# Optimization experiments

Hardware: AMD Instinct MI355X
Metric: run time of the kernel (lower is better)

Reference implementation:

```python
import jax, jax.numpy as jnp
import numpy as np

VOCAB = 1_000_000   # vocabulary_size
EMBED = 128         # embedding_size
BATCH = 4096
NUM_SAMPLED = 8192  # negative_samples


def setup_inputs() -> dict:
    key = jax.random.key(0)
    k1, k2, k3, k4 = jax.random.split(key, 4)
    predictions = jax.random.normal(k1, (BATCH, EMBED), dtype=jnp.float32)
    labels = jax.random.randint(k2, (BATCH, 1), 0, VOCAB, dtype=jnp.int64)
    # TF draws these via log_uniform_candidate_sampler; here they are fixed inputs.
    sampled_ids = jax.random.randint(k3, (NUM_SAMPLED,), 0, VOCAB, dtype=jnp.int64)
    W = jax.random.normal(k4, (VOCAB, EMBED), dtype=jnp.float32) * 0.05  # glorot-ish scale
    b = jnp.zeros((VOCAB,), dtype=jnp.float32)
    return {"predictions": predictions, "labels": labels,
            "sampled_ids": sampled_ids, "W": W, "b": b}


def _log_uniform_prob(ids, vocab):
    # P(k) = (log(k+2) - log(k+1)) / log(vocab+1), TF's log-uniform sampler.
    k = ids.astype(jnp.float32)
    return (jnp.log(k + 2.0) - jnp.log(k + 1.0)) / jnp.log(float(vocab) + 1.0)


def reference(predictions, labels, sampled_ids, W, b):
    lbl = labels[:, 0]                                   # [B]
    # --- true logits: gather one row per example ---
    true_w = W[lbl]                                      # [B, D] gather
    true_logits = jnp.sum(predictions * true_w, axis=-1) + b[lbl]
    true_logits = true_logits - jnp.log(NUM_SAMPLED * _log_uniform_prob(lbl, VOCAB))
    # --- sampled logits: gather S rows, small GEMM ---
    sampled_w = W[sampled_ids]                           # [S, D] gather
    sampled_logits = jnp.einsum('bd,sd->bs', predictions, sampled_w) + b[sampled_ids]
    sampled_logits = sampled_logits - jnp.log(NUM_SAMPLED * _log_uniform_prob(sampled_ids, VOCAB))
    # --- softmax cross-entropy with true class at column 0 ---
    logits = jnp.concatenate([true_logits[:, None], sampled_logits], axis=1)  # [B, 1+S]
    per_example_loss = -jax.nn.log_softmax(logits, axis=-1)[:, 0]
    return jnp.mean(per_example_loss)
```

## Files before the change

kernel.cpp:

```cpp
#include <hip/hip_runtime.h>
#include <hip/hip_bf16.h>
#include <math.h>

#define M 4096
#define N 8192
#define K 128
#define NSAMP 8192
#define VOCABF 1000000.0f

typedef __bf16 bf16x8 __attribute__((ext_vector_type(8)));
typedef float f32x16 __attribute__((ext_vector_type(16)));
typedef unsigned short u16x8 __attribute__((ext_vector_type(8)));

__device__ inline unsigned short f2bf(float f) {
    unsigned int u = __float_as_uint(f);
    unsigned int r = (u + 0x7FFFu + ((u >> 16) & 1u)) >> 16;
    return (unsigned short)r;
}

__global__ __launch_bounds__(256) void prep(const float* __restrict__ pred,
                                            const int* __restrict__ sampled,
                                            const float* __restrict__ W,
                                            const float* __restrict__ bias,
                                            unsigned short* __restrict__ Pb,
                                            unsigned short* __restrict__ Wsb,
                                            float* __restrict__ bcorr,
                                            float* __restrict__ rsum,
                                            float* __restrict__ out) {
    const int bx = blockIdx.x;
    if (bx < 256) {
        int t = bx * 256 + threadIdx.x;
        if (t < M) rsum[t] = 0.0f;
        if (t == 0) out[0] = 0.0f;
        int base = t * 8;
        float4 f0 = *(const float4*)(pred + base);
        float4 f1 = *(const float4*)(pred + base + 4);
        u16x8 v;
        v[0] = f2bf(f0.x); v[1] = f2bf(f0.y); v[2] = f2bf(f0.z); v[3] = f2bf(f0.w);
        v[4] = f2bf(f1.x); v[5] = f2bf(f1.y); v[6] = f2bf(f1.z); v[7] = f2bf(f1.w);
        *(u16x8*)(Pb + base) = v;
    } else {
        int t = (bx - 256) * 256 + threadIdx.x;
        int s = t >> 4, c = t & 15;
        int id = sampled[s];
        const float* src = W + (size_t)id * K + c * 8;
        float4 f0 = *(const float4*)src;
        float4 f1 = *(const float4*)(src + 4);
        u16x8 v;
        v[0] = f2bf(f0.x); v[1] = f2bf(f0.y); v[2] = f2bf(f0.z); v[3] = f2bf(f0.w);
        v[4] = f2bf(f1.x); v[5] = f2bf(f1.y); v[6] = f2bf(f1.z); v[7] = f2bf(f1.w);
        *(u16x8*)(Wsb + s * K + c * 8) = v;
        if (c == 0) {
            float kk = (float)id;
            float q = log1pf(1.0f / (kk + 1.0f)) / logf(VOCABF + 1.0f);
            bcorr[s] = bias[id] - logf((float)NSAMP * q);
        }
    }
}

__global__ __launch_bounds__(256, 4) void main_gemm(
        const unsigned short* __restrict__ Pb,
        const unsigned short* __restrict__ Wsb,
        const float* __restrict__ bcorr,
        float* __restrict__ row_sum) {
    const int tid  = threadIdx.x;
    const int lane = tid & 63;
    const int wid  = tid >> 6;
    const int l31  = lane & 31;
    const int half = lane >> 5;
    const int mrow = blockIdx.x * 128 + wid * 32 + l31;
    const int nb   = blockIdx.y * 256;

    bf16x8 a[8];
    const unsigned short* ap = Pb + (size_t)mrow * K + half * 8;
#pragma unroll
    for (int ks = 0; ks < 8; ++ks)
        a[ks] = *(const bf16x8*)(ap + ks * 16);

    float rs[16];
#pragma unroll
    for (int r = 0; r < 16; ++r) rs[r] = 0.0f;

#pragma unroll
    for (int t = 0; t < 8; ++t) {
        const int col = nb + t * 32 + l31;
        const float bc = bcorr[col];
        f32x16 acc;
#pragma unroll
        for (int r = 0; r < 16; ++r) acc[r] = bc;
        const unsigned short* bp = Wsb + (size_t)col * K + half * 8;
#pragma unroll
        for (int ks = 0; ks < 8; ++ks) {
            bf16x8 bf = *(const bf16x8*)(bp + ks * 16);
            acc = __builtin_amdgcn_mfma_f32_32x32x16_bf16(a[ks], bf, acc, 0, 0, 0);
        }
#pragma unroll
        for (int r = 0; r < 16; ++r) rs[r] += __expf(acc[r]);
    }

#pragma unroll
    for (int m = 1; m <= 16; m <<= 1) {
#pragma unroll
        for (int r = 0; r < 16; ++r) rs[r] += __shfl_xor(rs[r], m, 64);
    }
    if (l31 == 0) {
        const int rb = blockIdx.x * 128 + wid * 32 + 4 * half;
#pragma unroll
        for (int r = 0; r < 16; ++r) {
            int row = rb + (r & 3) + 8 * (r >> 2);
            atomicAdd(&row_sum[row], rs[r]);
        }
    }
}

__global__ __launch_bounds__(256) void finalize(const float* __restrict__ pred,
                                                const int* __restrict__ labels,
                                                const float* __restrict__ W,
                                                const float* __restrict__ bias,
                                                const float* __restrict__ row_sum,
                                                float* __restrict__ out) {
    __shared__ float part[16];
    int t = blockIdx.x * 256 + threadIdx.x;
    int row = t >> 4, c = t & 15;
    int id = labels[row];
    const float* wp = W + (size_t)id * K + c * 8;
    const float* pp = pred + (size_t)row * K + c * 8;
    float4 w0 = *(const float4*)wp, w1 = *(const float4*)(wp + 4);
    float4 p0 = *(const float4*)pp, p1 = *(const float4*)(pp + 4);
    float d = w0.x * p0.x + w0.y * p0.y + w0.z * p0.z + w0.w * p0.w
            + w1.x * p1.x + w1.y * p1.y + w1.z * p1.z + w1.w * p1.w;
#pragma unroll
    for (int m = 1; m <= 8; m <<= 1) d += __shfl_xor(d, m, 64);
    if (c == 0) {
        float kk = (float)id;
        float q = log1pf(1.0f / (kk + 1.0f)) / logf(VOCABF + 1.0f);
        float tl = d + bias[id] - logf((float)NSAMP * q);
        float loss = logf(row_sum[row] + __expf(tl)) - tl;
        part[threadIdx.x >> 4] = loss;
    }
    __syncthreads();
    if (threadIdx.x == 0) {
        float s = 0.0f;
#pragma unroll
        for (int i = 0; i < 16; ++i) s += part[i];
        atomicAdd(out, s * (1.0f / (float)M));
    }
}

extern "C" void kernel_launch(void* const* d_in, const int* in_sizes, int n_in,
                              void* d_out, int out_size, void* d_ws, size_t ws_size,
                              hipStream_t stream) {
    const float* pred    = (const float*)d_in[0];
    const int*   labels  = (const int*)d_in[1];
    const int*   sampled = (const int*)d_in[2];
    const float* W       = (const float*)d_in[3];
    const float* b       = (const float*)d_in[4];
    float* out = (float*)d_out;

    char* ws = (char*)d_ws;
    unsigned short* Wsb   = (unsigned short*)ws;
    unsigned short* Pb    = (unsigned short*)(ws + (1 << 21));
    float*          bcorr = (float*)(ws + (1 << 21) + (1 << 20));
    float*          rsum  = (float*)(ws + (1 << 21) + (1 << 20) + NSAMP * 4);

    prep<<<768, 256, 0, stream>>>(pred, sampled, W, b, Pb, Wsb, bcorr, rsum, out);
    main_gemm<<<dim3(32, 32), 256, 0, stream>>>(Pb, Wsb, bcorr, rsum);
    finalize<<<256, 256, 0, stream>>>(pred, labels, W, b, rsum, out);
}
```

Before: 594.6 us.

## Fuse prep into GEMM with double-buffered LDS staging and atomic-free partial sums

Removes the separate prep kernel. The GEMM now converts predictions to bf16 in registers and gathers the sampled W rows directly, staging them into swizzled, double-buffered shared memory with the bias correction computed per tile. Row-sum atomics are replaced by per-column-block partial writes that finalize reduces, which drops the zeroing pass. In exchange, each of the 32 column-block rows of workgroups re-gathers and re-converts the same W rows, and every workgroup converts its own copy of the prediction tile. There is also an extra barrier per tile iteration.

New measurement: 631.5 us. 1.06x slower.

```diff
diff --git a/kernel.cpp b/kernel.cpp
--- a/kernel.cpp
+++ b/kernel.cpp
@@ -3,9 +3,8 @@
 #include <math.h>
 
 #define M 4096
-#define N 8192
+#define NSAMP 8192
 #define K 128
-#define NSAMP 8192
 #define VOCABF 1000000.0f
 
 typedef __bf16 bf16x8 __attribute__((ext_vector_type(8)));
@@ -14,88 +13,102 @@
 
 __device__ inline unsigned short f2bf(float f) {
     unsigned int u = __float_as_uint(f);
-    unsigned int r = (u + 0x7FFFu + ((u >> 16) & 1u)) >> 16;
-    return (unsigned short)r;
+    return (unsigned short)((u + 0x7FFFu + ((u >> 16) & 1u)) >> 16);
 }
 
-__global__ __launch_bounds__(256) void prep(const float* __restrict__ pred,
-                                            const int* __restrict__ sampled,
-                                            const float* __restrict__ W,
-                                            const float* __restrict__ bias,
-                                            unsigned short* __restrict__ Pb,
-                                            unsigned short* __restrict__ Wsb,
-                                            float* __restrict__ bcorr,
-                                            float* __restrict__ rsum,
-                                            float* __restrict__ out) {
-    const int bx = blockIdx.x;
-    if (bx < 256) {
-        int t = bx * 256 + threadIdx.x;
-        if (t < M) rsum[t] = 0.0f;
-        if (t == 0) out[0] = 0.0f;
-        int base = t * 8;
-        float4 f0 = *(const float4*)(pred + base);
-        float4 f1 = *(const float4*)(pred + base + 4);
-        u16x8 v;
-        v[0] = f2bf(f0.x); v[1] = f2bf(f0.y); v[2] = f2bf(f0.z); v[3] = f2bf(f0.w);
-        v[4] = f2bf(f1.x); v[5] = f2bf(f1.y); v[6] = f2bf(f1.z); v[7] = f2bf(f1.w);
-        *(u16x8*)(Pb + base) = v;
-    } else {
-        int t = (bx - 256) * 256 + threadIdx.x;
-        int s = t >> 4, c = t & 15;
-        int id = sampled[s];
-        const float* src = W + (size_t)id * K + c * 8;
-        float4 f0 = *(const float4*)src;
-        float4 f1 = *(const float4*)(src + 4);
-        u16x8 v;
-        v[0] = f2bf(f0.x); v[1] = f2bf(f0.y); v[2] = f2bf(f0.z); v[3] = f2bf(f0.w);
-        v[4] = f2bf(f1.x); v[5] = f2bf(f1.y); v[6] = f2bf(f1.z); v[7] = f2bf(f1.w);
-        *(u16x8*)(Wsb + s * K + c * 8) = v;
-        if (c == 0) {
-            float kk = (float)id;
-            float q = log1pf(1.0f / (kk + 1.0f)) / logf(VOCABF + 1.0f);
-            bcorr[s] = bias[id] - logf((float)NSAMP * q);
-        }
-    }
+__device__ inline u16x8 pack8(float4 f0, float4 f1) {
+    u16x8 v;
+    v[0] = f2bf(f0.x); v[1] = f2bf(f0.y); v[2] = f2bf(f0.z); v[3] = f2bf(f0.w);
+    v[4] = f2bf(f1.x); v[5] = f2bf(f1.y); v[6] = f2bf(f1.z); v[7] = f2bf(f1.w);
+    return v;
+}
+__device__ inline bf16x8 as_bf(u16x8 u) {
+    union { u16x8 u; bf16x8 b; } cv; cv.u = u; return cv.b;
 }
 
-__global__ __launch_bounds__(256, 4) void main_gemm(
-        const unsigned short* __restrict__ Pb,
-        const unsigned short* __restrict__ Wsb,
-        const float* __restrict__ bcorr,
-        float* __restrict__ row_sum) {
+__global__ __launch_bounds__(256, 4) void fused_gemm(
+        const float* __restrict__ pred,
+        const int* __restrict__ sampled,
+        const float* __restrict__ W,
+        const float* __restrict__ bias,
+        float* __restrict__ partial,
+        float* __restrict__ out) {
+    __shared__ __align__(16) unsigned short Bt[2][32 * K];
+    __shared__ float Bc[2][32];
+
     const int tid  = threadIdx.x;
     const int lane = tid & 63;
     const int wid  = tid >> 6;
     const int l31  = lane & 31;
     const int half = lane >> 5;
-    const int mrow = blockIdx.x * 128 + wid * 32 + l31;
-    const int nb   = blockIdx.y * 256;
+    const int bx = blockIdx.x, by = blockIdx.y;
 
+    if (bx == 0 && by == 0 && tid == 0) out[0] = 0.0f;
+
+    const int mrow = bx * 128 + wid * 32 + l31;
     bf16x8 a[8];
-    const unsigned short* ap = Pb + (size_t)mrow * K + half * 8;
+    {
+        const float* ap = pred + (size_t)mrow * K + half * 8;
 #pragma unroll
-    for (int ks = 0; ks < 8; ++ks)
-        a[ks] = *(const bf16x8*)(ap + ks * 16);
+        for (int ks = 0; ks < 8; ++ks) {
+            float4 f0 = *(const float4*)(ap + ks * 16);
+            float4 f1 = *(const float4*)(ap + ks * 16 + 4);
+            a[ks] = as_bf(pack8(f0, f1));
+        }
+    }
+
+    const int scol = tid >> 3;
+    const int seg  = tid & 7;
+    float4 r0, r1, r2, r3; float bsv = 0.0f; int sid = 0;
+
+    auto LOAD = [&](int t) {
+        sid = sampled[by * 256 + t * 32 + scol];
+        const float4* src = (const float4*)(W + (size_t)sid * K + seg * 16);
+        r0 = src[0]; r1 = src[1]; r2 = src[2]; r3 = src[3];
+        if (seg == 0) bsv = bias[sid];
+    };
+    auto WRITE = [&](int b) {
+        u16x8 lo = pack8(r0, r1), hi = pack8(r2, r3);
+        const int swz = (scol & 15) << 4;
+        char* rowp = (char*)&Bt[b][scol * K];
+        const int o0 = seg * 32;
+        *(u16x8*)(rowp + ((o0)      ^ swz)) = lo;
+        *(u16x8*)(rowp + ((o0 + 16) ^ swz)) = hi;
+        if (seg == 0) {
+            float kk = (float)sid;
+            float q = log1pf(1.0f / (kk + 1.0f)) / logf(VOCABF + 1.0f);
+            Bc[b][scol] = bsv - logf((float)NSAMP * q);
+        }
+    };
 
     float rs[16];
 #pragma unroll
     for (int r = 0; r < 16; ++r) rs[r] = 0.0f;
 
+    LOAD(0); WRITE(0);
+    __syncthreads();
+
 #pragma unroll
     for (int t = 0; t < 8; ++t) {
-        const int col = nb + t * 32 + l31;
-        const float bc = bcorr[col];
+        const int cur = t & 1;
+        if (t < 7) LOAD(t + 1);
+
+        const float bc = Bc[cur][l31];
         f32x16 acc;
 #pragma unroll
         for (int r = 0; r < 16; ++r) acc[r] = bc;
-        const unsigned short* bp = Wsb + (size_t)col * K + half * 8;
+        const char* rowp = (const char*)&Bt[cur][l31 * K];
+        const int swz = (l31 & 15) << 4;
 #pragma unroll
         for (int ks = 0; ks < 8; ++ks) {
-            bf16x8 bf = *(const bf16x8*)(bp + ks * 16);
+            bf16x8 bf = *(const bf16x8*)(rowp + ((half * 16 + ks * 32) ^ swz));
             acc = __builtin_amdgcn_mfma_f32_32x32x16_bf16(a[ks], bf, acc, 0, 0, 0);
         }
 #pragma unroll
         for (int r = 0; r < 16; ++r) rs[r] += __expf(acc[r]);
+
+        if (t < 7) WRITE((t + 1) & 1);
+        __syncthreads();
     }
 
 #pragma unroll
@@ -104,11 +117,11 @@
         for (int r = 0; r < 16; ++r) rs[r] += __shfl_xor(rs[r], m, 64);
     }
     if (l31 == 0) {
-        const int rb = blockIdx.x * 128 + wid * 32 + 4 * half;
+        const int rb = bx * 128 + wid * 32 + 4 * half;
 #pragma unroll
         for (int r = 0; r < 16; ++r) {
             int row = rb + (r & 3) + 8 * (r >> 2);
-            atomicAdd(&row_sum[row], rs[r]);
+            partial[by * M + row] = rs[r];
         }
     }
 }
@@ -117,7 +130,7 @@
                                                 const int* __restrict__ labels,
                                                 const float* __restrict__ W,
                                                 const float* __restrict__ bias,
-                                                const float* __restrict__ row_sum,
+                                                const float* __restrict__ partial,
                                                 float* __restrict__ out) {
     __shared__ float part[16];
     int t = blockIdx.x * 256 + threadIdx.x;
@@ -129,21 +142,25 @@
     float4 p0 = *(const float4*)pp, p1 = *(const float4*)(pp + 4);
     float d = w0.x * p0.x + w0.y * p0.y + w0.z * p0.z + w0.w * p0.w
             + w1.x * p1.x + w1.y * p1.y + w1.z * p1.z + w1.w * p1.w;
+    float s = partial[c * M + row] + partial[(c + 16) * M + row];
 #pragma unroll
-    for (int m = 1; m <= 8; m <<= 1) d += __shfl_xor(d, m, 64);
+    for (int m = 1; m <= 8; m <<= 1) {
+        d += __shfl_xor(d, m, 64);
+        s += __shfl_xor(s, m, 64);
+    }
     if (c == 0) {
         float kk = (float)id;
         float q = log1pf(1.0f / (kk + 1.0f)) / logf(VOCABF + 1.0f);
         float tl = d + bias[id] - logf((float)NSAMP * q);
-        float loss = logf(row_sum[row] + __expf(tl)) - tl;
+        float loss = logf(s + __expf(tl)) - tl;
         part[threadIdx.x >> 4] = loss;
     }
     __syncthreads();
     if (threadIdx.x == 0) {
-        float s = 0.0f;
+        float sum = 0.0f;
 #pragma unroll
-        for (int i = 0; i < 16; ++i) s += part[i];
-        atomicAdd(out, s * (1.0f / (float)M));
+        for (int i = 0; i < 16; ++i) sum += part[i];
+        atomicAdd(out, sum * (1.0f / (float)M));
     }
 }
 
@@ -157,13 +174,8 @@
     const float* b       = (const float*)d_in[4];
     float* out = (float*)d_out;
 
-    char* ws = (char*)d_ws;
-    unsigned short* Wsb   = (unsigned short*)ws;
-    unsigned short* Pb    = (unsigned short*)(ws + (1 << 21));
-    float*          bcorr = (float*)(ws + (1 << 21) + (1 << 20));
-    float*          rsum  = (float*)(ws + (1 << 21) + (1 << 20) + NSAMP * 4);
+    float* partial = (float*)d_ws;
 
-    prep<<<768, 256, 0, stream>>>(pred, sampled, W, b, Pb, Wsb, bcorr, rsum, out);
-    main_gemm<<<dim3(32, 32), 256, 0, stream>>>(Pb, Wsb, bcorr, rsum);
-    finalize<<<256, 256, 0, stream>>>(pred, labels, W, b, rsum, out);
+    fused_gemm<<<dim3(32, 32), 256, 0, stream>>>(pred, sampled, W, b, partial, out);
+    finalize<<<256, 256, 0, stream>>>(pred, labels, W, b, partial, out);
 }
```

## Fuse pred conversion into GEMM, move true-logit into prep, replace atomics with partials

Applied to the files above, without the earlier changes.

Drops the separate bf16 conversion of predictions: the GEMM now loads fp32 predictions and converts them in registers. The true-logit dot product moves into the prep kernel alongside the sampled-row gather. Per-row atomicAdds in the GEMM are replaced by plain stores into a per-column-block partial buffer, which a smaller finalize kernel reduces. This removes atomic contention and the workspace round trip for the converted predictions, at the cost of twice the fp32 reads for A in the GEMM and a 32-way partial reduction.

Measured after the change: 597.5 us. No clear change (+0.5%).

```diff
diff --git a/kernel.cpp b/kernel.cpp
--- a/kernel.cpp
+++ b/kernel.cpp
@@ -3,9 +3,8 @@
 #include <math.h>
 
 #define M 4096
-#define N 8192
+#define NSAMP 8192
 #define K 128
-#define NSAMP 8192
 #define VOCABF 1000000.0f
 
 typedef __bf16 bf16x8 __attribute__((ext_vector_type(8)));
@@ -14,55 +13,69 @@
 
 __device__ inline unsigned short f2bf(float f) {
     unsigned int u = __float_as_uint(f);
-    unsigned int r = (u + 0x7FFFu + ((u >> 16) & 1u)) >> 16;
-    return (unsigned short)r;
+    return (unsigned short)((u + 0x7FFFu + ((u >> 16) & 1u)) >> 16);
+}
+
+__device__ inline u16x8 pack8(float4 f0, float4 f1) {
+    u16x8 v;
+    v[0] = f2bf(f0.x); v[1] = f2bf(f0.y); v[2] = f2bf(f0.z); v[3] = f2bf(f0.w);
+    v[4] = f2bf(f1.x); v[5] = f2bf(f1.y); v[6] = f2bf(f1.z); v[7] = f2bf(f1.w);
+    return v;
+}
+__device__ inline bf16x8 as_bf(u16x8 u) {
+    union { u16x8 u; bf16x8 b; } cv; cv.u = u; return cv.b;
 }
 
 __global__ __launch_bounds__(256) void prep(const float* __restrict__ pred,
+                                            const int* __restrict__ labels,
                                             const int* __restrict__ sampled,
                                             const float* __restrict__ W,
                                             const float* __restrict__ bias,
-                                            unsigned short* __restrict__ Pb,
                                             unsigned short* __restrict__ Wsb,
                                             float* __restrict__ bcorr,
-                                            float* __restrict__ rsum,
+                                            float* __restrict__ tl,
                                             float* __restrict__ out) {
+    const float inv_logv = 1.0f / logf(VOCABF + 1.0f);
     const int bx = blockIdx.x;
-    if (bx < 256) {
+    if (bx < 512) {
         int t = bx * 256 + threadIdx.x;
-        if (t < M) rsum[t] = 0.0f;
         if (t == 0) out[0] = 0.0f;
-        int base = t * 8;
-        float4 f0 = *(const float4*)(pred + base);
-        float4 f1 = *(const float4*)(pred + base + 4);
-        u16x8 v;
-        v[0] = f2bf(f0.x); v[1] = f2bf(f0.y); v[2] = f2bf(f0.z); v[3] = f2bf(f0.w);
-        v[4] = f2bf(f1.x); v[5] = f2bf(f1.y); v[6] = f2bf(f1.z); v[7] = f2bf(f1.w);
-        *(u16x8*)(Pb + base) = v;
-    } else {
-        int t = (bx - 256) * 256 + threadIdx.x;
         int s = t >> 4, c = t & 15;
         int id = sampled[s];
         const float* src = W + (size_t)id * K + c * 8;
         float4 f0 = *(const float4*)src;
         float4 f1 = *(const float4*)(src + 4);
-        u16x8 v;
-        v[0] = f2bf(f0.x); v[1] = f2bf(f0.y); v[2] = f2bf(f0.z); v[3] = f2bf(f0.w);
-        v[4] = f2bf(f1.x); v[5] = f2bf(f1.y); v[6] = f2bf(f1.z); v[7] = f2bf(f1.w);
-        *(u16x8*)(Wsb + s * K + c * 8) = v;
+        *(u16x8*)(Wsb + s * K + c * 8) = pack8(f0, f1);
         if (c == 0) {
             float kk = (float)id;
-            float q = log1pf(1.0f / (kk + 1.0f)) / logf(VOCABF + 1.0f);
+            float q = log1pf(1.0f / (kk + 1.0f)) * inv_logv;
             bcorr[s] = bias[id] - logf((float)NSAMP * q);
+        }
+    } else {
+        int t = (bx - 512) * 256 + threadIdx.x;
+        int row = t >> 4, c = t & 15;
+        int id = labels[row];
+        const float* wp = W + (size_t)id * K + c * 8;
+        const float* pp = pred + (size_t)row * K + c * 8;
+        float4 w0 = *(const float4*)wp, w1 = *(const float4*)(wp + 4);
+        float4 p0 = *(const float4*)pp, p1 = *(const float4*)(pp + 4);
+        float d = w0.x * p0.x + w0.y * p0.y + w0.z * p0.z + w0.w * p0.w
+                + w1.x * p1.x + w1.y * p1.y + w1.z * p1.z + w1.w * p1.w;
+#pragma unroll
+        for (int m = 1; m <= 8; m <<= 1) d += __shfl_xor(d, m, 64);
+        if (c == 0) {
+            float kk = (float)id;
+            float q = log1pf(1.0f / (kk + 1.0f)) * inv_logv;
+            tl[row] = d + bias[id] - logf((float)NSAMP * q);
         }
     }
 }
 
 __global__ __launch_bounds__(256, 4) void main_gemm(
-        const unsigned short* __restrict__ Pb,
+        const float* __restrict__ pred,
         const unsigned short* __restrict__ Wsb,
         const float* __restrict__ bcorr,
-        float* __restrict__ row_sum) {
+        float* __restrict__ partial) {
     const int tid  = threadIdx.x;
     const int lane = tid & 63;
     const int wid  = tid >> 6;
@@ -72,10 +85,15 @@
     const int nb   = blockIdx.y * 256;
 
     bf16x8 a[8];
-    const unsigned short* ap = Pb + (size_t)mrow * K + half * 8;
+    {
+        const float* ap = pred + (size_t)mrow * K + half * 8;
 #pragma unroll
-    for (int ks = 0; ks < 8; ++ks)
-        a[ks] = *(const bf16x8*)(ap + ks * 16);
+        for (int ks = 0; ks < 8; ++ks) {
+            float4 f0 = *(const float4*)(ap + ks * 16);
+            float4 f1 = *(const float4*)(ap + ks * 16 + 4);
+            a[ks] = as_bf(pack8(f0, f1));
+        }
+    }
 
     float rs[16];
 #pragma unroll
@@ -108,43 +126,27 @@
 #pragma unroll
         for (int r = 0; r < 16; ++r) {
             int row = rb + (r & 3) + 8 * (r >> 2);
-            atomicAdd(&row_sum[row], rs[r]);
+            partial[blockIdx.y * M + row] = rs[r];
         }
     }
 }
 
-__global__ __launch_bounds__(256) void finalize(const float* __restrict__ pred,
-                                                const int* __restrict__ labels,
-                                                const float* __restrict__ W,
-                                                const float* __restrict__ bias,
-                                                const float* __restrict__ row_sum,
+__global__ __launch_bounds__(256) void finalize(const float* __restrict__ partial,
+                                                const float* __restrict__ tl,
                                                 float* __restrict__ out) {
-    __shared__ float part[16];
-    int t = blockIdx.x * 256 + threadIdx.x;
-    int row = t >> 4, c = t & 15;
-    int id = labels[row];
-    const float* wp = W + (size_t)id * K + c * 8;
-    const float* pp = pred + (size_t)row * K + c * 8;
-    float4 w0 = *(const float4*)wp, w1 = *(const float4*)(wp + 4);
-    float4 p0 = *(const float4*)pp, p1 = *(const float4*)(pp + 4);
-    float d = w0.x * p0.x + w0.y * p0.y + w0.z * p0.z + w0.w * p0.w
-            + w1.x * p1.x + w1.y * p1.y + w1.z * p1.z + w1.w * p1.w;
+    __shared__ float wsum[4];
+    int row = blockIdx.x * 256 + threadIdx.x;
+    float s = 0.0f;
 #pragma unroll
-    for (int m = 1; m <= 8; m <<= 1) d += __shfl_xor(d, m, 64);
-    if (c == 0) {
-        float kk = (float)id;
-        float q = log1pf(1.0f / (kk + 1.0f)) / logf(VOCABF + 1.0f);
-        float tl = d + bias[id] - logf((float)NSAMP * q);
-        float loss = logf(row_sum[row] + __expf(tl)) - tl;
-        part[threadIdx.x >> 4] = loss;
-    }
+    for (int j = 0; j < 32; ++j) s += partial[j * M + row];
+    float t = tl[row];
+    float loss = logf(s + __expf(t)) - t;
+#pragma unroll
+    for (int m = 1; m <= 32; m <<= 1) loss += __shfl_xor(loss, m, 64);
+    if ((threadIdx.x & 63) == 0) wsum[threadIdx.x >> 6] = loss;
     __syncthreads();
-    if (threadIdx.x == 0) {
-        float s = 0.0f;
-#pragma unroll
-        for (int i = 0; i < 16; ++i) s += part[i];
-        atomicAdd(out, s * (1.0f / (float)M));
-    }
+    if (threadIdx.x == 0)
+        atomicAdd(out, (wsum[0] + wsum[1] + wsum[2] + wsum[3]) * (1.0f / (float)M));
 }
 
 extern "C" void kernel_launch(void* const* d_in, const int* in_sizes, int n_in,
@@ -159,11 +161,11 @@
 
     char* ws = (char*)d_ws;
     unsigned short* Wsb   = (unsigned short*)ws;
-    unsigned short* Pb    = (unsigned short*)(ws + (1 << 21));
-    float*          bcorr = (float*)(ws + (1 << 21) + (1 << 20));
-    float*          rsum  = (float*)(ws + (1 << 21) + (1 << 20) + NSAMP * 4);
+    float*          bcorr = (float*)(ws + (1 << 21));
+    float*          tl    = (float*)(ws + (1 << 21) + (1 << 15));
+    float*          part  = (float*)(ws + (1 << 21) + (1 << 15) + (1 << 14));
 
-    prep<<<768, 256, 0, stream>>>(pred, sampled, W, b, Pb, Wsb, bcorr, rsum, out);
-    main_gemm<<<dim3(32, 32), 256, 0, stream>>>(Pb, Wsb, bcorr, rsum);
-    finalize<<<256, 256, 0, stream>>>(pred, labels, W, b, rsum, out);
+    prep<<<768, 256, 0, stream>>>(pred, labels, sampled, W, b, Wsb, bcorr, tl, out);
+    main_gemm<<<dim3(32, 32), 256, 0, stream>>>(pred, Wsb, bcorr, part);
+    finalize<<<16, 256, 0, stream>>>(part, tl, out);
 }
```
